# Kernel tuning notes

Hardware: AMD Instinct MI355X
Metric: run time of the kernel (lower is better)

Reference implementation:

```python
import jax, jax.numpy as jnp
import numpy as np

B, H = 8192, 768


def _mk_linear(key, fan_in, fan_out):
    k1, k2 = jax.random.split(key)
    lim = 1.0 / np.sqrt(fan_in)
    W = jax.random.uniform(k1, (fan_out, fan_in), jnp.float32, -lim, lim)
    b = jax.random.uniform(k2, (fan_out,), jnp.float32, -lim, lim)
    return W, b


def setup_inputs() -> dict:
    key = jax.random.key(0)
    ks = jax.random.split(key, 6)
    modal_a = jax.random.normal(ks[0], (B, H), jnp.float32)
    modal_b = jax.random.normal(ks[1], (B, H), jnp.float32)
    W1m, b1m = _mk_linear(ks[2], H, H)
    W2m, b2m = _mk_linear(ks[3], H, H)
    W1v, b1v = _mk_linear(ks[4], H, H)
    W2v, b2v = _mk_linear(ks[5], H, H)
    return {"modal_a": modal_a, "modal_b": modal_b,
            "W1m": W1m, "b1m": b1m, "W2m": W2m, "b2m": b2m,
            "W1v": W1v, "b1v": b1v, "W2v": W2v, "b2v": b2v}


def reference(modal_a, modal_b, W1m, b1m, W2m, b2m, W1v, b1v, W2v, b2v):
    # mlp_mu: Linear -> Tanh -> Linear
    mu = jnp.tanh(modal_a @ W1m.T + b1m) @ W2m.T + b2m              # [B,H]
    # mlp_logvar: Linear -> Tanh -> Linear -> Tanh
    logvar = jnp.tanh(jnp.tanh(modal_a @ W1v.T + b1v) @ W2v.T + b2v)  # [B,H]
    inv_var = jnp.exp(-logvar)

    positive = -(mu - modal_b) ** 2 * 0.5 * inv_var                  # [B,H]

    # mean_j (mu[j] - mu[i])^2 = E[mu^2] - 2*mu[i]*E[mu] + mu[i]^2  (per feature dim)
    # Algebraic reduction of the O(B^2*H) tile in the original code.
    mu_mean = jnp.mean(mu, axis=0)                                   # [H]
    mu_sq_mean = jnp.mean(mu * mu, axis=0)                           # [H]
    pair_sq = mu_sq_mean - 2.0 * mu * mu_mean + mu * mu              # [B,H]
    negative = -pair_sq * 0.5 * inv_var                              # [B,H]

    pos_sum = jnp.sum(positive, axis=-1)                             # [B]
    neg_sum = jnp.sum(negative, axis=-1)                             # [B]
    lld = jnp.mean(pos_sum)
    bound = jnp.mean(pos_sum - neg_sum)
    return (lld, bound)
```

## Files before the change

kernel.cpp:

```cpp
#include <hip/hip_runtime.h>
#include <math.h>

typedef float v4f __attribute__((ext_vector_type(4)));
typedef short bf16x8 __attribute__((ext_vector_type(8)));

#define AS1 __attribute__((address_space(1)))
#define AS3 __attribute__((address_space(3)))

static constexpr int Bn = 8192;
static constexpr int Hn = 768;

__device__ __forceinline__ short f32_to_bf16(float x) {
    union { float f; unsigned u; } v; v.f = x;
    unsigned r = (v.u + 0x7FFFu + ((v.u >> 16) & 1u)) >> 16;
    return (short)r;
}

__global__ void prep_kernel(const float* __restrict__ A,
                            const float* __restrict__ W1m, const float* __restrict__ W2m,
                            const float* __restrict__ W1v, const float* __restrict__ W2v,
                            short* __restrict__ A_bf,
                            short* __restrict__ W1m_bf, short* __restrict__ W2m_bf,
                            short* __restrict__ W1v_bf, short* __restrict__ W2v_bf,
                            float* __restrict__ zbuf, int nzero) {
    const int tid = blockIdx.x * blockDim.x + threadIdx.x;
    if (tid < nzero) zbuf[tid] = 0.0f;
    constexpr int A4 = Bn * Hn / 4;
    constexpr int W4 = Hn * Hn / 4;
    const int total = A4 + 4 * W4;
    const int stride = gridDim.x * blockDim.x;
    for (int i = tid; i < total; i += stride) {
        const float* s; short* d; int j;
        if (i < A4) { s = A; d = A_bf; j = i; }
        else {
            int k = i - A4; int w = k / W4; j = k - w * W4;
            s = (w == 0) ? W1m : (w == 1) ? W2m : (w == 2) ? W1v : W2v;
            d = (w == 0) ? W1m_bf : (w == 1) ? W2m_bf : (w == 2) ? W1v_bf : W2v_bf;
        }
        float4 v = ((const float4*)s)[j];
        short4 o;
        o.x = f32_to_bf16(v.x); o.y = f32_to_bf16(v.y);
        o.z = f32_to_bf16(v.z); o.w = f32_to_bf16(v.w);
        ((short4*)d)[j] = o;
    }
}

template <int LAYER>
__global__ void gemm_fused(const short* __restrict__ A0, const short* __restrict__ A1,
                           const short* __restrict__ Wa, const short* __restrict__ Wb,
                           const float* __restrict__ ba, const float* __restrict__ bb,
                           void* __restrict__ outa, void* __restrict__ outb,
                           float* __restrict__ cs, float* __restrict__ cs2) {
    constexpr int K = Hn;
    __shared__ __align__(16) short As[128 * 64];
    __shared__ __align__(16) short Ws[128 * 64];

    const int z = blockIdx.z;
    const short* A = (LAYER == 1) ? A0 : (z ? A1 : A0);
    const short* W = z ? Wb : Wa;
    const float* bias = z ? bb : ba;
    void* out = z ? outb : outa;

    const int t = threadIdx.x;
    const int row0 = blockIdx.x * 128;
    const int col0 = blockIdx.y * 128;

    const int w = t >> 6, lane = t & 63;
    const int wm = w >> 1, wn = w & 1;
    const int lr = lane & 15, quad = lane >> 4;

    const int rt = t >> 3;
    const int bbk = t & 7;
    const int bsrc = bbk ^ (rt & 7);

    v4f acc[4][4] = {};

    for (int k0 = 0; k0 < K; k0 += 64) {
#pragma unroll
        for (int i = 0; i < 4; ++i) {
            const short* gA = A + (size_t)(row0 + i * 32 + rt) * K + k0 + bsrc * 8;
            const short* gW = W + (size_t)(col0 + i * 32 + rt) * K + k0 + bsrc * 8;
            __builtin_amdgcn_global_load_lds((AS1 void*)gA, (AS3 void*)&As[i * 2048 + t * 8], 16, 0, 0);
            __builtin_amdgcn_global_load_lds((AS1 void*)gW, (AS3 void*)&Ws[i * 2048 + t * 8], 16, 0, 0);
        }
        __syncthreads();
#pragma unroll
        for (int s = 0; s < 2; ++s) {
            const int kb = s * 4 + quad;
            bf16x8 af[4], bfr[4];
#pragma unroll
            for (int mt = 0; mt < 4; ++mt) {
                int m = wm * 64 + mt * 16 + lr;
                af[mt] = *(const bf16x8*)&As[m * 64 + ((kb ^ (m & 7)) << 3)];
            }
#pragma unroll
            for (int nt = 0; nt < 4; ++nt) {
                int n = wn * 64 + nt * 16 + lr;
                bfr[nt] = *(const bf16x8*)&Ws[n * 64 + ((kb ^ (n & 7)) << 3)];
            }
#pragma unroll
            for (int mt = 0; mt < 4; ++mt)
#pragma unroll
                for (int nt = 0; nt < 4; ++nt)
                    acc[mt][nt] = __builtin_amdgcn_mfma_f32_16x16x32_bf16(af[mt], bfr[nt], acc[mt][nt], 0, 0, 0);
        }
        __syncthreads();
    }

#pragma unroll
    for (int nt = 0; nt < 4; ++nt) {
        const int col = col0 + wn * 64 + nt * 16 + lr;
        const float bcol = bias[col];
        float s1 = 0.f, s2 = 0.f;
#pragma unroll
        for (int mt = 0; mt < 4; ++mt) {
#pragma unroll
            for (int r = 0; r < 4; ++r) {
                const int row = row0 + wm * 64 + mt * 16 + quad * 4 + r;
                float v = acc[mt][nt][r] + bcol;
                if (LAYER == 1) {
                    ((short*)out)[(size_t)row * Hn + col] = f32_to_bf16(tanhf(v));
                } else if (LAYER == 2) {
                    if (z == 0) {
                        ((float*)out)[(size_t)row * Hn + col] = v;
                        s1 += v; s2 += v * v;
                    } else {
                        ((float*)out)[(size_t)row * Hn + col] = expf(-tanhf(v));
                    }
                }
            }
        }
        if (LAYER == 2 && z == 0) {
            s1 += __shfl_xor(s1, 16); s1 += __shfl_xor(s1, 32);
            s2 += __shfl_xor(s2, 16); s2 += __shfl_xor(s2, 32);
            if (quad == 0) {
                atomicAdd(&cs[col], s1);
                atomicAdd(&cs2[col], s2);
            }
        }
    }
}

__global__ void final_reduce(const float* __restrict__ mu, const float* __restrict__ iv,
                             const float* __restrict__ mb, const float* __restrict__ cs,
                             const float* __restrict__ cs2, float* __restrict__ accum,
                             float* __restrict__ out) {
    constexpr float invB = 1.0f / 8192.0f;
    const int tid = blockIdx.x * blockDim.x + threadIdx.x;
    const int stride = gridDim.x * blockDim.x;
    const int total4 = Bn * Hn / 4;
    float s0 = 0.f, s1 = 0.f;
    for (int i = tid; i < total4; i += stride) {
        const int c4 = i % (Hn / 4);
        float4 m4 = ((const float4*)mu)[i];
        float4 v4 = ((const float4*)iv)[i];
        float4 b4 = ((const float4*)mb)[i];
        float4 c1 = ((const float4*)cs)[c4];
        float4 c2 = ((const float4*)cs2)[c4];
        const float mm[4] = {c1.x, c1.y, c1.z, c1.w};
        const float ms[4] = {c2.x, c2.y, c2.z, c2.w};
        const float m_[4] = {m4.x, m4.y, m4.z, m4.w};
        const float v_[4] = {v4.x, v4.y, v4.z, v4.w};
        const float b_[4] = {b4.x, b4.y, b4.z, b4.w};
#pragma unroll
        for (int j = 0; j < 4; ++j) {
            float mean  = mm[j] * invB;
            float sqm   = ms[j] * invB;
            float d     = m_[j] - b_[j];
            float pos   = -0.5f * d * d * v_[j];
            float pq    = sqm - 2.f * m_[j] * mean + m_[j] * m_[j];
            float neg   = -0.5f * pq * v_[j];
            s0 += pos;
            s1 += pos - neg;
        }
    }
    const int lane = threadIdx.x & 63, w = threadIdx.x >> 6;
    for (int off = 32; off > 0; off >>= 1) {
        s0 += __shfl_down(s0, off);
        s1 += __shfl_down(s1, off);
    }
    __shared__ float r0[4], r1[4];
    if (lane == 0) { r0[w] = s0; r1[w] = s1; }
    __syncthreads();
    if (threadIdx.x == 0) {
        atomicAdd(&accum[0], r0[0] + r0[1] + r0[2] + r0[3]);
        atomicAdd(&accum[1], r1[0] + r1[1] + r1[2] + r1[3]);
        __threadfence();
        unsigned old = atomicAdd((unsigned int*)&accum[3], 1u);
        if (old == gridDim.x - 1) {
            float a0 = atomicAdd(&accum[0], 0.0f);
            float a1 = atomicAdd(&accum[1], 0.0f);
            out[0] = a0 * invB;
            out[1] = a1 * invB;
        }
    }
}

extern "C" void kernel_launch(void* const* d_in, const int* in_sizes, int n_in,
                              void* d_out, int out_size, void* d_ws, size_t ws_size,
                              hipStream_t stream) {
    const float* modal_a = (const float*)d_in[0];
    const float* modal_b = (const float*)d_in[1];
    const float* W1m = (const float*)d_in[2];
    const float* b1m = (const float*)d_in[3];
    const float* W2m = (const float*)d_in[4];
    const float* b2m = (const float*)d_in[5];
    const float* W1v = (const float*)d_in[6];
    const float* b1v = (const float*)d_in[7];
    const float* W2v = (const float*)d_in[8];
    const float* b2v = (const float*)d_in[9];
    float* out = (float*)d_out;

    char* ws = (char*)d_ws;
    constexpr size_t szAH = (size_t)Bn * Hn * 2;
    constexpr size_t szW  = (size_t)Hn * Hn * 2;
    constexpr size_t szMF = (size_t)Bn * Hn * 4;
    short* A_bf   = (short*)(ws);
    short* h1m    = (short*)(ws + szAH);
    short* h1v    = (short*)(ws + 2 * szAH);
    short* W1m_bf = (short*)(ws + 3 * szAH);
    short* W2m_bf = (short*)(ws + 3 * szAH + szW);
    short* W1v_bf = (short*)(ws + 3 * szAH + 2 * szW);
    short* W2v_bf = (short*)(ws + 3 * szAH + 3 * szW);
    float* mu     = (float*)(ws + 3 * szAH + 4 * szW);
    float* iv     = (float*)(ws + 3 * szAH + 4 * szW + szMF);
    float* cs     = (float*)(ws + 3 * szAH + 4 * szW + 2 * szMF);
    float* cs2    = cs + Hn;
    float* accum  = cs2 + Hn;

    prep_kernel<<<1280, 256, 0, stream>>>(modal_a, W1m, W2m, W1v, W2v,
                                          A_bf, W1m_bf, W2m_bf, W1v_bf, W2v_bf,
                                          cs, 2 * Hn + 4);

    dim3 grid(Bn / 128, Hn / 128, 2);
    gemm_fused<1><<<grid, 256, 0, stream>>>(A_bf, A_bf, W1m_bf, W1v_bf, b1m, b1v,
                                            h1m, h1v, nullptr, nullptr);

    gemm_fused<2><<<grid, 256, 0, stream>>>(h1m, h1v, W2m_bf, W2v_bf, b2m, b2v,
                                            mu, iv, cs, cs2);

    final_reduce<<<768, 256, 0, stream>>>(mu, iv, modal_b, cs, cs2, accum, out);
}
```

Before: 206.7 us.

## Fuse loss reduction into second GEMM epilogue and pair mu/logvar GEMMs per block

The final reduction kernel is folded into the layer-2 GEMM epilogue. Per-column sums of mu, mu^2, inv_var and inv_var*mu are accumulated atomically, and the negative term is expanded algebraically so a tiny combine kernel can finish it. This removes writing and re-reading the full fp32 mu and inv_var tensors. Each block now computes both the mu and logvar branches on 64x64 tiles with a shared A tile in layer 1, and uses a fast exp-based tanh. The costs are more atomics, smaller tiles with less reuse per MFMA, and float accumulation-order and approximation differences.

```diff
diff --git a/kernel.cpp b/kernel.cpp
--- a/kernel.cpp
+++ b/kernel.cpp
@@ -9,11 +9,19 @@
 
 static constexpr int Bn = 8192;
 static constexpr int Hn = 768;
+static constexpr float invB = 1.0f / 8192.0f;
 
 __device__ __forceinline__ short f32_to_bf16(float x) {
     union { float f; unsigned u; } v; v.f = x;
     unsigned r = (v.u + 0x7FFFu + ((v.u >> 16) & 1u)) >> 16;
     return (short)r;
+}
+
+__device__ __forceinline__ float fast_tanh(float x) {
+    float xc = fminf(fmaxf(x, -15.0f), 15.0f);
+    float e = __expf(2.0f * xc);
+    float r = __builtin_amdgcn_rcpf(e + 1.0f);
+    return 1.0f - 2.0f * r;
 }
 
 __global__ void prep_kernel(const float* __restrict__ A,
@@ -46,153 +54,168 @@
 }
 
 template <int LAYER>
-__global__ void gemm_fused(const short* __restrict__ A0, const short* __restrict__ A1,
-                           const short* __restrict__ Wa, const short* __restrict__ Wb,
-                           const float* __restrict__ ba, const float* __restrict__ bb,
-                           void* __restrict__ outa, void* __restrict__ outb,
-                           float* __restrict__ cs, float* __restrict__ cs2) {
+__launch_bounds__(256, 5)
+__global__ void gemm_club(const short* __restrict__ Am_g, const short* __restrict__ Av_g,
+                          const short* __restrict__ Wm_g, const short* __restrict__ Wv_g,
+                          const float* __restrict__ bm, const float* __restrict__ bv,
+                          short* __restrict__ outm, short* __restrict__ outv,
+                          const float* __restrict__ mb,
+                          float* __restrict__ cs, float* __restrict__ cs2,
+                          float* __restrict__ siv, float* __restrict__ sivmu,
+                          float* __restrict__ accum) {
     constexpr int K = Hn;
-    __shared__ __align__(16) short As[128 * 64];
-    __shared__ __align__(16) short Ws[128 * 64];
-
-    const int z = blockIdx.z;
-    const short* A = (LAYER == 1) ? A0 : (z ? A1 : A0);
-    const short* W = z ? Wb : Wa;
-    const float* bias = z ? bb : ba;
-    void* out = z ? outb : outa;
+    constexpr int NSH = (LAYER == 1) ? 3 * 4096 : 4 * 4096;
+    __shared__ __align__(16) short smem[NSH];
+    short* As_m = smem;
+    short* As_v = (LAYER == 1) ? smem : smem + 4096;
+    short* Ws_m = (LAYER == 1) ? smem + 4096 : smem + 8192;
+    short* Ws_v = (LAYER == 1) ? smem + 8192 : smem + 12288;
 
     const int t = threadIdx.x;
-    const int row0 = blockIdx.x * 128;
-    const int col0 = blockIdx.y * 128;
-
+    const int row0 = blockIdx.x * 64;
+    const int col0 = blockIdx.y * 64;
     const int w = t >> 6, lane = t & 63;
     const int wm = w >> 1, wn = w & 1;
     const int lr = lane & 15, quad = lane >> 4;
 
     const int rt = t >> 3;
-    const int bbk = t & 7;
-    const int bsrc = bbk ^ (rt & 7);
-
-    v4f acc[4][4] = {};
+    const int bsrc = (t & 7) ^ (rt & 7);
+
+    const short* pAm[2]; const short* pAv[2]; const short* pWm[2]; const short* pWv[2];
+#pragma unroll
+    for (int i = 0; i < 2; ++i) {
+        pAm[i] = Am_g + (size_t)(row0 + i * 32 + rt) * K + bsrc * 8;
+        pWm[i] = Wm_g + (size_t)(col0 + i * 32 + rt) * K + bsrc * 8;
+        pWv[i] = Wv_g + (size_t)(col0 + i * 32 + rt) * K + bsrc * 8;
+        pAv[i] = (LAYER == 2) ? (Av_g + (size_t)(row0 + i * 32 + rt) * K + bsrc * 8) : pAm[i];
+    }
+
+    v4f accm[2][2] = {}, accv[2][2] = {};
 
     for (int k0 = 0; k0 < K; k0 += 64) {
 #pragma unroll
-        for (int i = 0; i < 4; ++i) {
-            const short* gA = A + (size_t)(row0 + i * 32 + rt) * K + k0 + bsrc * 8;
-            const short* gW = W + (size_t)(col0 + i * 32 + rt) * K + k0 + bsrc * 8;
-            __builtin_amdgcn_global_load_lds((AS1 void*)gA, (AS3 void*)&As[i * 2048 + t * 8], 16, 0, 0);
-            __builtin_amdgcn_global_load_lds((AS1 void*)gW, (AS3 void*)&Ws[i * 2048 + t * 8], 16, 0, 0);
+        for (int i = 0; i < 2; ++i) {
+            __builtin_amdgcn_global_load_lds((AS1 void*)pAm[i], (AS3 void*)&As_m[i * 2048 + t * 8], 16, 0, 0);
+            if (LAYER == 2)
+                __builtin_amdgcn_global_load_lds((AS1 void*)pAv[i], (AS3 void*)&As_v[i * 2048 + t * 8], 16, 0, 0);
+            __builtin_amdgcn_global_load_lds((AS1 void*)pWm[i], (AS3 void*)&Ws_m[i * 2048 + t * 8], 16, 0, 0);
+            __builtin_amdgcn_global_load_lds((AS1 void*)pWv[i], (AS3 void*)&Ws_v[i * 2048 + t * 8], 16, 0, 0);
+            pAm[i] += 64; pWm[i] += 64; pWv[i] += 64;
+            if (LAYER == 2) pAv[i] += 64;
         }
         __syncthreads();
 #pragma unroll
         for (int s = 0; s < 2; ++s) {
             const int kb = s * 4 + quad;
-            bf16x8 af[4], bfr[4];
-#pragma unroll
-            for (int mt = 0; mt < 4; ++mt) {
-                int m = wm * 64 + mt * 16 + lr;
-                af[mt] = *(const bf16x8*)&As[m * 64 + ((kb ^ (m & 7)) << 3)];
-            }
-#pragma unroll
-            for (int nt = 0; nt < 4; ++nt) {
-                int n = wn * 64 + nt * 16 + lr;
-                bfr[nt] = *(const bf16x8*)&Ws[n * 64 + ((kb ^ (n & 7)) << 3)];
-            }
-#pragma unroll
-            for (int mt = 0; mt < 4; ++mt)
-#pragma unroll
-                for (int nt = 0; nt < 4; ++nt)
-                    acc[mt][nt] = __builtin_amdgcn_mfma_f32_16x16x32_bf16(af[mt], bfr[nt], acc[mt][nt], 0, 0, 0);
+            bf16x8 am[2], av[2], bmf[2], bvf[2];
+#pragma unroll
+            for (int mt = 0; mt < 2; ++mt) {
+                int m = wm * 32 + mt * 16 + lr;
+                int off = m * 64 + ((kb ^ (m & 7)) << 3);
+                am[mt] = *(const bf16x8*)&As_m[off];
+                if (LAYER == 2) av[mt] = *(const bf16x8*)&As_v[off];
+            }
+#pragma unroll
+            for (int nt = 0; nt < 2; ++nt) {
+                int n = wn * 32 + nt * 16 + lr;
+                int off = n * 64 + ((kb ^ (n & 7)) << 3);
+                bmf[nt] = *(const bf16x8*)&Ws_m[off];
+                bvf[nt] = *(const bf16x8*)&Ws_v[off];
+            }
+#pragma unroll
+            for (int mt = 0; mt < 2; ++mt)
+#pragma unroll
+                for (int nt = 0; nt < 2; ++nt) {
+                    accm[mt][nt] = __builtin_amdgcn_mfma_f32_16x16x32_bf16(am[mt], bmf[nt], accm[mt][nt], 0, 0, 0);
+                    accv[mt][nt] = __builtin_amdgcn_mfma_f32_16x16x32_bf16(
+                        (LAYER == 1) ? am[mt] : av[mt], bvf[nt], accv[mt][nt], 0, 0, 0);
+                }
         }
         __syncthreads();
     }
 
-#pragma unroll
-    for (int nt = 0; nt < 4; ++nt) {
-        const int col = col0 + wn * 64 + nt * 16 + lr;
-        const float bcol = bias[col];
-        float s1 = 0.f, s2 = 0.f;
-#pragma unroll
-        for (int mt = 0; mt < 4; ++mt) {
-#pragma unroll
-            for (int r = 0; r < 4; ++r) {
-                const int row = row0 + wm * 64 + mt * 16 + quad * 4 + r;
-                float v = acc[mt][nt][r] + bcol;
-                if (LAYER == 1) {
-                    ((short*)out)[(size_t)row * Hn + col] = f32_to_bf16(tanhf(v));
-                } else if (LAYER == 2) {
-                    if (z == 0) {
-                        ((float*)out)[(size_t)row * Hn + col] = v;
-                        s1 += v; s2 += v * v;
-                    } else {
-                        ((float*)out)[(size_t)row * Hn + col] = expf(-tanhf(v));
-                    }
+    if (LAYER == 1) {
+#pragma unroll
+        for (int nt = 0; nt < 2; ++nt) {
+            const int col = col0 + wn * 32 + nt * 16 + lr;
+            const float bmc = bm[col], bvc = bv[col];
+#pragma unroll
+            for (int mt = 0; mt < 2; ++mt) {
+#pragma unroll
+                for (int r = 0; r < 4; ++r) {
+                    const int row = row0 + wm * 32 + mt * 16 + quad * 4 + r;
+                    outm[(size_t)row * Hn + col] = f32_to_bf16(fast_tanh(accm[mt][nt][r] + bmc));
+                    outv[(size_t)row * Hn + col] = f32_to_bf16(fast_tanh(accv[mt][nt][r] + bvc));
                 }
             }
         }
-        if (LAYER == 2 && z == 0) {
-            s1 += __shfl_xor(s1, 16); s1 += __shfl_xor(s1, 32);
-            s2 += __shfl_xor(s2, 16); s2 += __shfl_xor(s2, 32);
+    } else {
+        float pos = 0.f, q = 0.f;
+#pragma unroll
+        for (int nt = 0; nt < 2; ++nt) {
+            const int col = col0 + wn * 32 + nt * 16 + lr;
+            const float bmc = bm[col], bvc = bv[col];
+            float c1 = 0.f, c2 = 0.f, c3 = 0.f, c4 = 0.f;
+#pragma unroll
+            for (int mt = 0; mt < 2; ++mt) {
+#pragma unroll
+                for (int r = 0; r < 4; ++r) {
+                    const int row = row0 + wm * 32 + mt * 16 + quad * 4 + r;
+                    float mu = accm[mt][nt][r] + bmc;
+                    float tv = fast_tanh(accv[mt][nt][r] + bvc);
+                    float iv = __expf(-tv);
+                    float mbv = mb[(size_t)row * Hn + col];
+                    float d = mu - mbv;
+                    pos += iv * d * d;
+                    q   += iv * mu * mu;
+                    c1 += mu; c2 += mu * mu; c3 += iv; c4 += iv * mu;
+                }
+            }
+            c1 += __shfl_xor(c1, 16); c1 += __shfl_xor(c1, 32);
+            c2 += __shfl_xor(c2, 16); c2 += __shfl_xor(c2, 32);
+            c3 += __shfl_xor(c3, 16); c3 += __shfl_xor(c3, 32);
+            c4 += __shfl_xor(c4, 16); c4 += __shfl_xor(c4, 32);
             if (quad == 0) {
-                atomicAdd(&cs[col], s1);
-                atomicAdd(&cs2[col], s2);
-            }
-        }
-    }
-}
-
-__global__ void final_reduce(const float* __restrict__ mu, const float* __restrict__ iv,
-                             const float* __restrict__ mb, const float* __restrict__ cs,
-                             const float* __restrict__ cs2, float* __restrict__ accum,
-                             float* __restrict__ out) {
-    constexpr float invB = 1.0f / 8192.0f;
-    const int tid = blockIdx.x * blockDim.x + threadIdx.x;
-    const int stride = gridDim.x * blockDim.x;
-    const int total4 = Bn * Hn / 4;
-    float s0 = 0.f, s1 = 0.f;
-    for (int i = tid; i < total4; i += stride) {
-        const int c4 = i % (Hn / 4);
-        float4 m4 = ((const float4*)mu)[i];
-        float4 v4 = ((const float4*)iv)[i];
-        float4 b4 = ((const float4*)mb)[i];
-        float4 c1 = ((const float4*)cs)[c4];
-        float4 c2 = ((const float4*)cs2)[c4];
-        const float mm[4] = {c1.x, c1.y, c1.z, c1.w};
-        const float ms[4] = {c2.x, c2.y, c2.z, c2.w};
-        const float m_[4] = {m4.x, m4.y, m4.z, m4.w};
-        const float v_[4] = {v4.x, v4.y, v4.z, v4.w};
-        const float b_[4] = {b4.x, b4.y, b4.z, b4.w};
-#pragma unroll
-        for (int j = 0; j < 4; ++j) {
-            float mean  = mm[j] * invB;
-            float sqm   = ms[j] * invB;
-            float d     = m_[j] - b_[j];
-            float pos   = -0.5f * d * d * v_[j];
-            float pq    = sqm - 2.f * m_[j] * mean + m_[j] * m_[j];
-            float neg   = -0.5f * pq * v_[j];
-            s0 += pos;
-            s1 += pos - neg;
-        }
-    }
-    const int lane = threadIdx.x & 63, w = threadIdx.x >> 6;
-    for (int off = 32; off > 0; off >>= 1) {
-        s0 += __shfl_down(s0, off);
-        s1 += __shfl_down(s1, off);
-    }
-    __shared__ float r0[4], r1[4];
-    if (lane == 0) { r0[w] = s0; r1[w] = s1; }
+                atomicAdd(&cs[col], c1);
+                atomicAdd(&cs2[col], c2);
+                atomicAdd(&siv[col], c3);
+                atomicAdd(&sivmu[col], c4);
+            }
+        }
+        for (int off = 32; off > 0; off >>= 1) {
+            pos += __shfl_down(pos, off);
+            q   += __shfl_down(q, off);
+        }
+        __shared__ float redP[4], redQ[4];
+        if (lane == 0) { redP[w] = pos; redQ[w] = q; }
+        __syncthreads();
+        if (t == 0) {
+            atomicAdd(&accum[0], redP[0] + redP[1] + redP[2] + redP[3]);
+            atomicAdd(&accum[1], redQ[0] + redQ[1] + redQ[2] + redQ[3]);
+        }
+    }
+}
+
+__global__ void combine_kernel(const float* __restrict__ cs, const float* __restrict__ cs2,
+                               const float* __restrict__ siv, const float* __restrict__ sivmu,
+                               const float* __restrict__ accum, float* __restrict__ out) {
+    const int h = threadIdx.x;
+    float term = siv[h] * cs2[h] - 2.0f * sivmu[h] * cs[h];
+    for (int off = 32; off > 0; off >>= 1) term += __shfl_down(term, off);
+    __shared__ float red[12];
+    const int lane = h & 63, w = h >> 6;
+    if (lane == 0) red[w] = term;
     __syncthreads();
-    if (threadIdx.x == 0) {
-        atomicAdd(&accum[0], r0[0] + r0[1] + r0[2] + r0[3]);
-        atomicAdd(&accum[1], r1[0] + r1[1] + r1[2] + r1[3]);
-        __threadfence();
-        unsigned old = atomicAdd((unsigned int*)&accum[3], 1u);
-        if (old == gridDim.x - 1) {
-            float a0 = atomicAdd(&accum[0], 0.0f);
-            float a1 = atomicAdd(&accum[1], 0.0f);
-            out[0] = a0 * invB;
-            out[1] = a1 * invB;
-        }
+    if (h == 0) {
+        float T = 0.f;
+#pragma unroll
+        for (int i = 0; i < 12; ++i) T += red[i];
+        float P = accum[0];
+        float Q = accum[1];
+        float pos_sum = -0.5f * P;
+        float neg_sum = -0.5f * (T * invB + Q);
+        out[0] = pos_sum * invB;
+        out[1] = (pos_sum - neg_sum) * invB;
     }
 }
 
@@ -214,7 +237,6 @@
     char* ws = (char*)d_ws;
     constexpr size_t szAH = (size_t)Bn * Hn * 2;
     constexpr size_t szW  = (size_t)Hn * Hn * 2;
-    constexpr size_t szMF = (size_t)Bn * Hn * 4;
     short* A_bf   = (short*)(ws);
     short* h1m    = (short*)(ws + szAH);
     short* h1v    = (short*)(ws + 2 * szAH);
@@ -222,22 +244,24 @@
     short* W2m_bf = (short*)(ws + 3 * szAH + szW);
     short* W1v_bf = (short*)(ws + 3 * szAH + 2 * szW);
     short* W2v_bf = (short*)(ws + 3 * szAH + 3 * szW);
-    float* mu     = (float*)(ws + 3 * szAH + 4 * szW);
-    float* iv     = (float*)(ws + 3 * szAH + 4 * szW + szMF);
-    float* cs     = (float*)(ws + 3 * szAH + 4 * szW + 2 * szMF);
+    float* cs     = (float*)(ws + 3 * szAH + 4 * szW);
     float* cs2    = cs + Hn;
-    float* accum  = cs2 + Hn;
+    float* siv    = cs + 2 * Hn;
+    float* sivmu  = cs + 3 * Hn;
+    float* accum  = cs + 4 * Hn;
 
     prep_kernel<<<1280, 256, 0, stream>>>(modal_a, W1m, W2m, W1v, W2v,
                                           A_bf, W1m_bf, W2m_bf, W1v_bf, W2v_bf,
-                                          cs, 2 * Hn + 4);
-
-    dim3 grid(Bn / 128, Hn / 128, 2);
-    gemm_fused<1><<<grid, 256, 0, stream>>>(A_bf, A_bf, W1m_bf, W1v_bf, b1m, b1v,
-                                            h1m, h1v, nullptr, nullptr);
-
-    gemm_fused<2><<<grid, 256, 0, stream>>>(h1m, h1v, W2m_bf, W2v_bf, b2m, b2v,
-                                            mu, iv, cs, cs2);
-
-    final_reduce<<<768, 256, 0, stream>>>(mu, iv, modal_b, cs, cs2, accum, out);
-}
+                                          cs, 4 * Hn + 2);
+
+    dim3 grid(Bn / 64, Hn / 64);
+    gemm_club<1><<<grid, 256, 0, stream>>>(A_bf, A_bf, W1m_bf, W1v_bf, b1m, b1v,
+                                           h1m, h1v, nullptr,
+                                           nullptr, nullptr, nullptr, nullptr, nullptr);
+
+    gemm_club<2><<<grid, 256, 0, stream>>>(h1m, h1v, W2m_bf, W2v_bf, b2m, b2v,
+                                           nullptr, nullptr, modal_b,
+                                           cs, cs2, siv, sivmu, accum);
+
+    combine_kernel<<<1, 768, 0, stream>>>(cs, cs2, siv, sivmu, accum, out);
+}
```

Measured after the change: 197.3 us. -4.6%, faster.
